# Kernel tuning notes

Hardware: AMD Instinct MI355X
Metric: run time of the kernel (lower is better)

## Reference

```python
import jax, jax.numpy as jnp
import numpy as np

DIM = 2048
NHEAD = 16
HEAD_DIM = DIM // NHEAD
FF_HIDDEN = 5632
EPS = 1e-6


def setup_inputs() -> dict:
    key = jax.random.key(0)
    ks = jax.random.split(key, 8)
    B, S = 2, 2048
    sd = 0.02
    return {
        "x": jax.random.normal(ks[0], (B, S, DIM), dtype=jnp.float32),
        "w_qkv": jax.random.normal(ks[1], (DIM, 3 * DIM), dtype=jnp.float32) * sd,
        "w_out": jax.random.normal(ks[2], (DIM, DIM), dtype=jnp.float32) * sd,
        "g1": jnp.ones((DIM,), dtype=jnp.float32),
        "g2": jnp.ones((DIM,), dtype=jnp.float32),
        "w1": jax.random.normal(ks[3], (DIM, FF_HIDDEN), dtype=jnp.float32) * sd,
        "w3": jax.random.normal(ks[4], (DIM, FF_HIDDEN), dtype=jnp.float32) * sd,
        "w2": jax.random.normal(ks[5], (FF_HIDDEN, DIM), dtype=jnp.float32) * sd,
    }


def _rmsnorm(x, g):
    rms = jnp.sqrt(jnp.mean(x * x, axis=-1, keepdims=True) + EPS)
    return x / rms * g


def _attention(x, w_qkv, w_out):
    B, S, D = x.shape
    qkv = x @ w_qkv  # [B,S,3D]
    q, k, v = jnp.split(qkv, 3, axis=-1)
    # [B,H,S,hd]
    q = q.reshape(B, S, NHEAD, HEAD_DIM).transpose(0, 2, 1, 3)
    k = k.reshape(B, S, NHEAD, HEAD_DIM).transpose(0, 2, 1, 3)
    v = v.reshape(B, S, NHEAD, HEAD_DIM).transpose(0, 2, 1, 3)
    scores = jnp.einsum("bhqd,bhkd->bhqk", q, k) / jnp.sqrt(jnp.float32(HEAD_DIM))
    causal = jnp.tril(jnp.ones((S, S), dtype=bool))
    scores = jnp.where(causal, scores, -jnp.inf)
    attn = jax.nn.softmax(scores, axis=-1)
    out = jnp.einsum("bhqk,bhkd->bhqd", attn, v)
    out = out.transpose(0, 2, 1, 3).reshape(B, S, D)
    return out @ w_out


def _swiglu(x, w1, w3, w2):
    return (jax.nn.silu(x @ w1) * (x @ w3)) @ w2


def reference(x, w_qkv, w_out, g1, g2, w1, w3, w2):
    x = x + _attention(_rmsnorm(x, g1), w_qkv, w_out)
    x = x + _swiglu(_rmsnorm(x, g2), w1, w3, w2)
    return x
```

## Files before the change

kernel.cpp:

```cpp
#include <hip/hip_runtime.h>
#include <hip/hip_bf16.h>
#include <stdint.h>


typedef __attribute__((ext_vector_type(8))) short bf16x8;
typedef __attribute__((ext_vector_type(8))) unsigned short u16x8;
typedef __attribute__((ext_vector_type(4))) float f32x4;

__device__ __forceinline__ unsigned short f2bf(float f) {
  union { float f; unsigned int u; } c; c.f = f;
  unsigned int u = c.u + 0x7fffu + ((c.u >> 16) & 1u);
  return (unsigned short)(u >> 16);
}
__device__ __forceinline__ float bf2f(unsigned short h) {
  union { unsigned int u; float f; } c; c.u = ((unsigned int)h) << 16;
  return c.f;
}

__device__ __forceinline__ void gload16(const void* g, void* l) {
  __builtin_amdgcn_global_load_lds(
      (const __attribute__((address_space(1))) void*)g,
      (__attribute__((address_space(3))) void*)l, 16, 0, 0);
}

__global__ __launch_bounds__(256)
void rmsnorm_bf16(const float* __restrict__ x, const float* __restrict__ g,
                  unsigned short* __restrict__ y)
{
  const long row = blockIdx.x;
  const float* xr = x + row * 2048;
  const int t = threadIdx.x;
  float4 a = *(const float4*)(xr + t * 8);
  float4 b = *(const float4*)(xr + t * 8 + 4);
  float ss = a.x*a.x + a.y*a.y + a.z*a.z + a.w*a.w
           + b.x*b.x + b.y*b.y + b.z*b.z + b.w*b.w;
#pragma unroll
  for (int off = 32; off >= 1; off >>= 1) ss += __shfl_xor(ss, off, 64);
  __shared__ float sm[4];
  if ((t & 63) == 0) sm[t >> 6] = ss;
  __syncthreads();
  float inv = rsqrtf((sm[0] + sm[1] + sm[2] + sm[3]) * (1.0f / 2048.0f) + 1e-6f);
  float4 ga = *(const float4*)(g + t * 8);
  float4 gb = *(const float4*)(g + t * 8 + 4);
  u16x8 ov;
  ov[0] = f2bf(a.x * inv * ga.x); ov[1] = f2bf(a.y * inv * ga.y);
  ov[2] = f2bf(a.z * inv * ga.z); ov[3] = f2bf(a.w * inv * ga.w);
  ov[4] = f2bf(b.x * inv * gb.x); ov[5] = f2bf(b.y * inv * gb.y);
  ov[6] = f2bf(b.z * inv * gb.z); ov[7] = f2bf(b.w * inv * gb.w);
  *(u16x8*)(y + row * 2048 + t * 8) = ov;
}

__global__ __launch_bounds__(256)
void rmsnorm_bf16_in(const unsigned short* __restrict__ x, const float* __restrict__ g,
                     unsigned short* __restrict__ y)
{
  const long row = blockIdx.x;
  const unsigned short* xr = x + row * 2048;
  const int t = threadIdx.x;
  u16x8 iv = *(const u16x8*)(xr + t * 8);
  float v[8];
  float ss = 0.f;
#pragma unroll
  for (int j = 0; j < 8; j++) { v[j] = bf2f(iv[j]); ss += v[j] * v[j]; }
#pragma unroll
  for (int off = 32; off >= 1; off >>= 1) ss += __shfl_xor(ss, off, 64);
  __shared__ float sm[4];
  if ((t & 63) == 0) sm[t >> 6] = ss;
  __syncthreads();
  float inv = rsqrtf((sm[0] + sm[1] + sm[2] + sm[3]) * (1.0f / 2048.0f) + 1e-6f);
  float4 ga = *(const float4*)(g + t * 8);
  float4 gb = *(const float4*)(g + t * 8 + 4);
  u16x8 ov;
  ov[0] = f2bf(v[0] * inv * ga.x); ov[1] = f2bf(v[1] * inv * ga.y);
  ov[2] = f2bf(v[2] * inv * ga.z); ov[3] = f2bf(v[3] * inv * ga.w);
  ov[4] = f2bf(v[4] * inv * gb.x); ov[5] = f2bf(v[5] * inv * gb.y);
  ov[6] = f2bf(v[6] * inv * gb.z); ov[7] = f2bf(v[7] * inv * gb.w);
  *(u16x8*)(y + row * 2048 + t * 8) = ov;
}

__global__ __launch_bounds__(256)
void transpose_w(const float* __restrict__ in, unsigned short* __restrict__ outp,
                 int K, int N)
{
  __shared__ unsigned short tile[64 * 64];
  const int n0 = blockIdx.x * 64, k0 = blockIdx.y * 64;
  const int tid = threadIdx.x;
#pragma unroll
  for (int p = 0; p < 4; p++) {
    int f = tid + p * 256;
    int row = f >> 4, c4 = f & 15;
    float4 v = *(const float4*)(in + (long)(k0 + row) * N + n0 + c4 * 4);
    ushort4 o;
    o.x = f2bf(v.x); o.y = f2bf(v.y); o.z = f2bf(v.z); o.w = f2bf(v.w);
    *(ushort4*)((char*)tile + row * 128
                + (((c4 >> 1) ^ (row >> 3)) * 16) + (c4 & 1) * 8) = o;
  }
  __syncthreads();
#pragma unroll
  for (int q = 0; q < 2; q++) {
    int idx = tid + q * 256;
    int nl = idx >> 3, l8 = idx & 7;
    u16x8 o;
#pragma unroll
    for (int j = 0; j < 8; j++) {
      int kl = l8 * 8 + j;
      o[j] = *(const unsigned short*)((char*)tile + kl * 128
               + (((nl >> 3) ^ (kl >> 3)) * 16) + (nl & 7) * 2);
    }
    *(u16x8*)(outp + (long)(n0 + nl) * K + k0 + l8 * 8) = o;
  }
}

template<int EPI>
__global__ __launch_bounds__(256)
void gemm_bt(const unsigned short* __restrict__ A,
             const unsigned short* __restrict__ Bt,
             void* __restrict__ Cout,
             const float* __restrict__ res,
             const unsigned short* __restrict__ mulsrc,
             unsigned short* __restrict__ vTout,
             int M, int N, int K)
{
  __shared__ unsigned short lds[2 * 128 * 64];
  const int tid = threadIdx.x;
  const int lane = tid & 63, wave = tid >> 6;
  const int wr = wave >> 1, wc = wave & 1;
  const int l15 = lane & 15, lg = lane >> 4;

  const int nwg = gridDim.x * gridDim.y;
  int wg = blockIdx.y * gridDim.x + blockIdx.x;
  wg = (wg & 7) * (nwg >> 3) + (wg >> 3);
  const int bx = wg % gridDim.x, by = wg / gridDim.x;
  const long m0 = (long)by * 128, n0 = (long)bx * 128;

  f32x4 acc[4][4];
#pragma unroll
  for (int m = 0; m < 4; m++)
#pragma unroll
    for (int n = 0; n < 4; n++) acc[m][n] = f32x4{0.f, 0.f, 0.f, 0.f};

  const int rsub = lane >> 3;
  const int csw = (lane & 7) ^ rsub;
  const unsigned short* Ab = A + (m0 + wave * 32 + rsub) * (long)K + csw * 8;
  const unsigned short* Bb = Bt + (n0 + wave * 32 + rsub) * (long)K + csw * 8;
  unsigned short* Al = lds + wave * 2048;
  unsigned short* Bl = lds + 8192 + wave * 2048;

  for (int kt = 0; kt < K; kt += 64) {
    __syncthreads();
#pragma unroll
    for (int i = 0; i < 4; i++) {
      gload16(Ab + (long)(i * 8) * K + kt, Al + i * 512);
      gload16(Bb + (long)(i * 8) * K + kt, Bl + i * 512);
    }
    __syncthreads();
#pragma unroll
    for (int kc = 0; kc < 2; kc++) {
      bf16x8 af[4], bfr[4];
#pragma unroll
      for (int m = 0; m < 4; m++) {
        int row = wr * 64 + m * 16 + l15;
        int off = row * 128 + ((kc * 64 + lg * 16) ^ ((row & 7) << 4));
        af[m] = *(const bf16x8*)((const char*)lds + off);
      }
#pragma unroll
      for (int n = 0; n < 4; n++) {
        int row = wc * 64 + n * 16 + l15;
        int off = 16384 + row * 128 + ((kc * 64 + lg * 16) ^ ((row & 7) << 4));
        bfr[n] = *(const bf16x8*)((const char*)lds + off);
      }
#pragma unroll
      for (int m = 0; m < 4; m++)
#pragma unroll
        for (int n = 0; n < 4; n++)
          acc[m][n] = __builtin_amdgcn_mfma_f32_16x16x32_bf16(af[m], bfr[n], acc[m][n], 0, 0, 0);
    }
  }

  if (EPI == 3) {
#pragma unroll
    for (int m = 0; m < 4; m++)
#pragma unroll
      for (int n = 0; n < 4; n++)
#pragma unroll
        for (int r = 0; r < 4; r++) {
          long row = m0 + wr * 64 + m * 16 + lg * 4 + r;
          long col = n0 + wc * 64 + n * 16 + l15;
          ((float*)Cout)[row * N + col] = acc[m][n][r] + res[row * N + col];
        }
    return;
  }

  __syncthreads();
  unsigned short* Cl = lds;
#pragma unroll
  for (int m = 0; m < 4; m++)
#pragma unroll
    for (int n = 0; n < 4; n++)
#pragma unroll
      for (int r = 0; r < 4; r++) {
        float v = acc[m][n][r];
        if (EPI == 1) v = v / (1.f + __expf(-v));
        int row = wr * 64 + m * 16 + lg * 4 + r;
        int col = wc * 64 + n * 16 + l15;
        Cl[row * 128 + (((col >> 3) ^ (row >> 3)) & 15) * 8 + (col & 7)] = f2bf(v);
      }
  __syncthreads();
#pragma unroll
  for (int r8 = 0; r8 < 8; r8++) {
    int id = tid + r8 * 256;
    int row = id >> 4, c = (id & 15) * 8;
    int ch = (id & 15) ^ (row >> 3);
    long grow = m0 + row, gcol = n0 + c;
    u16x8 v = *(const u16x8*)(Cl + row * 128 + ch * 8);
    if (EPI == 2) {
      u16x8 mm = *(const u16x8*)(mulsrc + grow * N + gcol);
#pragma unroll
      for (int j = 0; j < 8; j++) v[j] = f2bf(bf2f(v[j]) * bf2f(mm[j]));
    }
    *(u16x8*)((unsigned short*)Cout + grow * N + gcol) = v;
  }

  if (EPI == 0 && vTout != nullptr && n0 >= 4096) {
    const int hh = (int)((n0 - 4096) >> 7);
    const int b = (int)(m0 >> 11);
    const long s0 = m0 & 2047;
    unsigned short* vtb = vTout + ((long)(b * 16 + hh) * 128) * 2048;
#pragma unroll
    for (int r8 = 0; r8 < 8; r8++) {
      int id = tid + r8 * 256;
      int d = id >> 4, sc = (id & 15) * 8;
      int ch = ((d >> 3) ^ (id & 15)) & 15;
      u16x8 v;
#pragma unroll
      for (int j = 0; j < 8; j++) v[j] = Cl[(sc + j) * 128 + ch * 8 + (d & 7)];
      *(u16x8*)(vtb + (long)d * 2048 + s0 + sc) = v;
    }
  }
}

template<int EPI>
__global__ __launch_bounds__(256)
void gemm_mt64(const unsigned short* __restrict__ A,
               const unsigned short* __restrict__ Bt,
               void* __restrict__ Cout,
               const float* __restrict__ res,
               const unsigned short* __restrict__ res16,
               int M, int N, int K)
{
  __shared__ unsigned short lds[64 * 64 + 128 * 64];
  const int tid = threadIdx.x;
  const int lane = tid & 63, wave = tid >> 6;
  const int wr = wave >> 1, wc = wave & 1;
  const int l15 = lane & 15, lg = lane >> 4;

  const int nwg = gridDim.x * gridDim.y;
  int wg = blockIdx.y * gridDim.x + blockIdx.x;
  wg = (wg & 7) * (nwg >> 3) + (wg >> 3);
  const int bx = wg % gridDim.x, by = wg / gridDim.x;
  const long m0 = (long)by * 64, n0 = (long)bx * 128;

  f32x4 acc[2][4];
#pragma unroll
  for (int m = 0; m < 2; m++)
#pragma unroll
    for (int n = 0; n < 4; n++) acc[m][n] = f32x4{0.f, 0.f, 0.f, 0.f};

  const int rsub = lane >> 3;
  const int csw = (lane & 7) ^ rsub;
  const unsigned short* Ab = A + (m0 + wave * 16 + rsub) * (long)K + csw * 8;
  const unsigned short* Bb = Bt + (n0 + wave * 32 + rsub) * (long)K + csw * 8;
  unsigned short* Al = lds + wave * 1024;
  unsigned short* Bl = lds + 4096 + wave * 2048;

  for (int kt = 0; kt < K; kt += 64) {
    __syncthreads();
#pragma unroll
    for (int i = 0; i < 2; i++)
      gload16(Ab + (long)(i * 8) * K + kt, Al + i * 512);
#pragma unroll
    for (int i = 0; i < 4; i++)
      gload16(Bb + (long)(i * 8) * K + kt, Bl + i * 512);
    __syncthreads();
#pragma unroll
    for (int kc = 0; kc < 2; kc++) {
      bf16x8 af[2], bfr[4];
#pragma unroll
      for (int m = 0; m < 2; m++) {
        int row = wr * 32 + m * 16 + l15;
        int off = row * 128 + ((kc * 64 + lg * 16) ^ ((row & 7) << 4));
        af[m] = *(const bf16x8*)((const char*)lds + off);
      }
#pragma unroll
      for (int n = 0; n < 4; n++) {
        int row = wc * 64 + n * 16 + l15;
        int off = 8192 + row * 128 + ((kc * 64 + lg * 16) ^ ((row & 7) << 4));
        bfr[n] = *(const bf16x8*)((const char*)lds + off);
      }
#pragma unroll
      for (int m = 0; m < 2; m++)
#pragma unroll
        for (int n = 0; n < 4; n++)
          acc[m][n] = __builtin_amdgcn_mfma_f32_16x16x32_bf16(af[m], bfr[n], acc[m][n], 0, 0, 0);
    }
  }

  if (EPI == 5) {
#pragma unroll
    for (int m = 0; m < 2; m++)
#pragma unroll
      for (int n = 0; n < 4; n++)
#pragma unroll
        for (int r = 0; r < 4; r++) {
          long row = m0 + wr * 32 + m * 16 + lg * 4 + r;
          long col = n0 + wc * 64 + n * 16 + l15;
          ((float*)Cout)[row * N + col] = acc[m][n][r] + bf2f(res16[row * N + col]);
        }
    return;
  }

  __syncthreads();
  unsigned short* Cl = lds;
#pragma unroll
  for (int m = 0; m < 2; m++)
#pragma unroll
    for (int n = 0; n < 4; n++)
#pragma unroll
      for (int r = 0; r < 4; r++) {
        int row = wr * 32 + m * 16 + lg * 4 + r;
        int col = wc * 64 + n * 16 + l15;
        float v = acc[m][n][r] + res[(m0 + row) * N + n0 + col];
        Cl[row * 128 + (((col >> 3) ^ (row >> 3)) & 15) * 8 + (col & 7)] = f2bf(v);
      }
  __syncthreads();
#pragma unroll
  for (int rnd = 0; rnd < 4; rnd++) {
    int id = tid + rnd * 256;
    int row = id >> 4, c = (id & 15) * 8;
    int ch = (id & 15) ^ (row >> 3);
    u16x8 v = *(const u16x8*)(Cl + row * 128 + ch * 8);
    *(u16x8*)((unsigned short*)Cout + (m0 + row) * N + n0 + c) = v;
  }
}

#define QSTEP(qf, mrow, lrow, o, qb, isdiag) do {                              \
    f32x4 sacc[4];                                                             \
    __builtin_amdgcn_s_setprio(1);                                             \
    _Pragma("unroll")                                                          \
    for (int cg = 0; cg < 4; cg++) {                                           \
      f32x4 a = f32x4{0.f, 0.f, 0.f, 0.f};                                     \
      _Pragma("unroll")                                                        \
      for (int kc = 0; kc < 4; kc++) {                                         \
        int krow = cg * 16 + l15;                                              \
        bf16x8 kf = *(const bf16x8*)((char*)Klds +                             \
            (krow * 256 + ((kc * 64 + lg * 16) ^ ((krow & 7) << 4))));         \
        a = __builtin_amdgcn_mfma_f32_16x16x32_bf16(qf[kc], kf, a, 0, 0, 0);   \
      }                                                                        \
      sacc[cg] = a;                                                            \
    }                                                                          \
    __builtin_amdgcn_s_setprio(0);                                             \
    float p[4][4], pm[4];                                                      \
    _Pragma("unroll")                                                          \
    for (int r = 0; r < 4; r++) pm[r] = -1e30f;                                \
    _Pragma("unroll")                                                          \
    for (int cg = 0; cg < 4; cg++)                                             \
      _Pragma("unroll")                                                        \
      for (int r = 0; r < 4; r++) {                                            \
        float v = sacc[cg][r] * scale;                                         \
        if (isdiag) {                                                          \
          int kvg = kv0 + cg * 16 + l15;                                       \
          int qg = qb + w * 16 + lg * 4 + r;                                   \
          if (kvg > qg) v = -1e30f;                                            \
        }                                                                      \
        p[cg][r] = v;                                                          \
        pm[r] = fmaxf(pm[r], v);                                               \
      }                                                                        \
    _Pragma("unroll")                                                          \
    for (int r = 0; r < 4; r++) {                                              \
      _Pragma("unroll")                                                        \
      for (int off = 1; off < 16; off <<= 1)                                   \
        pm[r] = fmaxf(pm[r], __shfl_xor(pm[r], off, 64));                      \
      float mn = fmaxf(mrow[r], pm[r]);                                        \
      float al = __expf(mrow[r] - mn);                                         \
      mrow[r] = mn;                                                            \
      float s = 0.f;                                                           \
      _Pragma("unroll")                                                        \
      for (int cg = 0; cg < 4; cg++) { p[cg][r] = __expf(p[cg][r] - mn); s += p[cg][r]; } \
      _Pragma("unroll")                                                        \
      for (int off = 1; off < 16; off <<= 1)                                   \
        s += __shfl_xor(s, off, 64);                                           \
      lrow[r] = lrow[r] * al + s;                                              \
      _Pragma("unroll")                                                        \
      for (int dg = 0; dg < 8; dg++) o[dg][r] *= al;                           \
    }                                                                          \
    _Pragma("unroll")                                                          \
    for (int cg = 0; cg < 4; cg++)                                             \
      _Pragma("unroll")                                                        \
      for (int r = 0; r < 4; r++) {                                            \
        int q = lg * 4 + r;                                                    \
        *((unsigned short*)((char*)&Plds[w][0] +                               \
            (q * 128 + (((cg * 16 + l15) * 2) ^ ((q & 7) << 4))))) = f2bf(p[cg][r]); \
      }                                                                        \
    asm volatile("s_waitcnt lgkmcnt(0)" ::: "memory");                         \
    __builtin_amdgcn_sched_barrier(0);                                         \
    __builtin_amdgcn_s_setprio(1);                                             \
    _Pragma("unroll")                                                          \
    for (int kc = 0; kc < 2; kc++) {                                           \
      bf16x8 pa = *(const bf16x8*)((char*)&Plds[w][0] +                        \
          (l15 * 128 + ((kc * 64 + lg * 16) ^ ((l15 & 7) << 4))));             \
      _Pragma("unroll")                                                        \
      for (int dg = 0; dg < 8; dg++) {                                         \
        int d = dg * 16 + l15;                                                 \
        bf16x8 vf = *(const bf16x8*)((char*)Vlds +                             \
            (d * 128 + ((kc * 64 + lg * 16) ^ ((d & 7) << 4))));               \
        o[dg] = __builtin_amdgcn_mfma_f32_16x16x32_bf16(pa, vf, o[dg], 0, 0, 0); \
      }                                                                        \
    }                                                                          \
    __builtin_amdgcn_s_setprio(0);                                             \
  } while (0)

__global__ __launch_bounds__(256, 2)
void attn_fwd(const unsigned short* __restrict__ qkv,
              const unsigned short* __restrict__ vT,
              unsigned short* __restrict__ out)
{
  __shared__ unsigned short Klds[64 * 128];
  __shared__ unsigned short Vlds[128 * 64];
  __shared__ unsigned short Plds[4][16 * 64];
  const int tid = threadIdx.x, lane = tid & 63, w = tid >> 6;
  const int l15 = lane & 15, lg = lane >> 4;

  const int nwg = gridDim.x * gridDim.y;
  int wg = blockIdx.y * gridDim.x + blockIdx.x;
  wg = (wg & 7) * (nwg >> 3) + (wg >> 3);
  const int ip = wg % 16;
  const int bh = wg / 16;
  const int b = bh >> 4, hh = bh & 15;

  const int qbA = ip * 64, qbB = (31 - ip) * 64;
  const long base = (long)b * 2048 * 6144;
  const int qoff = hh * 128, koff = 2048 + hh * 128;
  const unsigned short* vTg = vT + (long)bh * (128 * 2048);

  bf16x8 qfA[4], qfB[4];
  {
    long qrA = qbA + w * 16 + l15, qrB = qbB + w * 16 + l15;
#pragma unroll
    for (int kc = 0; kc < 4; kc++) {
      qfA[kc] = *(const bf16x8*)(qkv + base + qrA * 6144 + qoff + kc * 32 + lg * 8);
      qfB[kc] = *(const bf16x8*)(qkv + base + qrB * 6144 + qoff + kc * 32 + lg * 8);
    }
  }
  f32x4 oA[8], oB[8];
#pragma unroll
  for (int dg = 0; dg < 8; dg++) {
    oA[dg] = f32x4{0.f, 0.f, 0.f, 0.f};
    oB[dg] = f32x4{0.f, 0.f, 0.f, 0.f};
  }
  float mA[4] = {-1e30f, -1e30f, -1e30f, -1e30f}, lA[4] = {0.f, 0.f, 0.f, 0.f};
  float mB[4] = {-1e30f, -1e30f, -1e30f, -1e30f}, lB[4] = {0.f, 0.f, 0.f, 0.f};
  const float scale = 0.08838834764831845f;

  const int s_st = tid >> 4, d0 = (tid & 15) * 8;
  const int vrow = tid >> 3, vc = tid & 7;

  const int nt = 32 - ip;
  for (int t = 0; t < nt; t++) {
    const int kv0 = t * 64;
#pragma unroll
    for (int u = 0; u < 4; u++) {
      int srow = s_st + u * 16;
      uint4 kk = *(const uint4*)(qkv + base + (long)(kv0 + srow) * 6144 + koff + d0);
      *(uint4*)((char*)Klds + (srow * 256 + ((d0 * 2) ^ ((srow & 7) << 4)))) = kk;
    }
#pragma unroll
    for (int u = 0; u < 4; u++) {
      int d = vrow + u * 32;
      uint4 vv = *(const uint4*)(vTg + (long)d * 2048 + kv0 + vc * 8);
      *(uint4*)((char*)Vlds + (d * 128 + ((vc * 16) ^ ((d & 7) << 4)))) = vv;
    }
    __syncthreads();

    if (t <= ip) QSTEP(qfA, mA, lA, oA, qbA, (t == ip));
    QSTEP(qfB, mB, lB, oB, qbB, (t == nt - 1));

    __syncthreads();
  }

#pragma unroll
  for (int r = 0; r < 4; r++) {
    float invA = 1.f / lA[r], invB = 1.f / lB[r];
    long rowA = (long)b * 2048 + qbA + w * 16 + lg * 4 + r;
    long rowB = (long)b * 2048 + qbB + w * 16 + lg * 4 + r;
#pragma unroll
    for (int dg = 0; dg < 8; dg++) {
      out[rowA * 2048 + hh * 128 + dg * 16 + l15] = f2bf(oA[dg][r] * invA);
      out[rowB * 2048 + hh * 128 + dg * 16 + l15] = f2bf(oB[dg][r] * invB);
    }
  }
}

extern "C" void kernel_launch(void* const* d_in, const int* in_sizes, int n_in,
                              void* d_out, int out_size, void* d_ws, size_t ws_size,
                              hipStream_t stream)
{
  const float* x     = (const float*)d_in[0];
  const float* w_qkv = (const float*)d_in[1];
  const float* w_out = (const float*)d_in[2];
  const float* g1    = (const float*)d_in[3];
  const float* g2    = (const float*)d_in[4];
  const float* w1    = (const float*)d_in[5];
  const float* w3    = (const float*)d_in[6];
  const float* w2    = (const float*)d_in[7];
  float* outp = (float*)d_out;
  char* ws = (char*)d_ws;

  unsigned short* wT  = (unsigned short*)(ws);
  unsigned short* y   = (unsigned short*)(ws + 25165824);
  unsigned short* qkv = (unsigned short*)(ws + 41943040);
  unsigned short* att = (unsigned short*)(ws + 92274688);
  unsigned short* x1b = (unsigned short*)(ws + 109051904);
  unsigned short* s1  = (unsigned short*)(ws + 142606336);
  unsigned short* vTb = s1;
  unsigned short* h   = qkv;

  rmsnorm_bf16<<<4096, 256, 0, stream>>>(x, g1, y);
  transpose_w<<<dim3(96, 32), 256, 0, stream>>>(w_qkv, wT, 2048, 6144);
  gemm_bt<0><<<dim3(48, 32), 256, 0, stream>>>(y, wT, qkv, nullptr, nullptr, vTb, 4096, 6144, 2048);
  attn_fwd<<<dim3(16, 32), 256, 0, stream>>>(qkv, vTb, att);
  transpose_w<<<dim3(32, 32), 256, 0, stream>>>(w_out, wT, 2048, 2048);
  gemm_mt64<4><<<dim3(16, 64), 256, 0, stream>>>(att, wT, x1b, x, nullptr, 4096, 2048, 2048);

  rmsnorm_bf16_in<<<4096, 256, 0, stream>>>(x1b, g2, y);
  transpose_w<<<dim3(88, 32), 256, 0, stream>>>(w1, wT, 2048, 5632);
  gemm_bt<1><<<dim3(44, 32), 256, 0, stream>>>(y, wT, s1, nullptr, nullptr, nullptr, 4096, 5632, 2048);
  transpose_w<<<dim3(88, 32), 256, 0, stream>>>(w3, wT, 2048, 5632);
  gemm_bt<2><<<dim3(44, 32), 256, 0, stream>>>(y, wT, h, nullptr, s1, nullptr, 4096, 5632, 2048);
  transpose_w<<<dim3(32, 88), 256, 0, stream>>>(w2, wT, 5632, 2048);
  gemm_mt64<5><<<dim3(16, 64), 256, 0, stream>>>(h, wT, outp, nullptr, x1b, 4096, 2048, 5632);
}
```

Baseline: 702.6 us.

## Replace 128x128 GEMM with 256x256 eight-wave double-buffered pipelined GEMM

Replaces the 128x128 single-buffered gemm_bt with a 256x256-tile, 512-thread kernel that double-buffers A and B in 128KB LDS. It interleaves global-to-LDS loads with MFMA phases using explicit barriers, waitcnts, sched_barriers and setprio. The goal is to hide global load latency and raise arithmetic intensity for the QKV, w1 and w3 GEMMs. In exchange it runs at one workgroup per CU with a large register footprint, and the smaller grids (384 and 352 blocks) may not balance evenly across CUs.

```diff
diff --git a/kernel.cpp b/kernel.cpp
--- a/kernel.cpp
+++ b/kernel.cpp
@@ -111,108 +111,146 @@
   }
 }
 
+#define PH_BAR __builtin_amdgcn_s_barrier()
+#define SB0 __builtin_amdgcn_sched_barrier(0)
+#define LGKM0 asm volatile("s_waitcnt lgkmcnt(0)" ::: "memory")
+#define VM4 asm volatile("s_waitcnt vmcnt(4)" ::: "memory");
+#define VM0 asm volatile("s_waitcnt vmcnt(0)" ::: "memory");
+
+#define STGA(RBASE, h, t) { \
+  gload16(Asb + (long)((h) * 128) * K + (t) * 64, L + (RBASE) + wave * 1024); \
+  gload16(Asb + (long)((h) * 128 + 64) * K + (t) * 64, L + (RBASE) + 8192 + wave * 1024); }
+#define STGB(RBASE, h, t) { \
+  gload16(Bsb + (long)((h) * 128) * K + (t) * 64, L + (RBASE) + wave * 1024); \
+  gload16(Bsb + (long)((h) * 128 + 64) * K + (t) * 64, L + (RBASE) + 8192 + wave * 1024); }
+
+#define LDB8(RBASE) { \
+  bfr0[0] = *(const bf16x8*)(L + (RBASE) + bbase + 0 * 2048 + k0off); \
+  bfr1[0] = *(const bf16x8*)(L + (RBASE) + bbase + 0 * 2048 + k1off); \
+  bfr0[1] = *(const bf16x8*)(L + (RBASE) + bbase + 1 * 2048 + k0off); \
+  bfr1[1] = *(const bf16x8*)(L + (RBASE) + bbase + 1 * 2048 + k1off); \
+  bfr0[2] = *(const bf16x8*)(L + (RBASE) + bbase + 2 * 2048 + k0off); \
+  bfr1[2] = *(const bf16x8*)(L + (RBASE) + bbase + 2 * 2048 + k1off); \
+  bfr0[3] = *(const bf16x8*)(L + (RBASE) + bbase + 3 * 2048 + k0off); \
+  bfr1[3] = *(const bf16x8*)(L + (RBASE) + bbase + 3 * 2048 + k1off); }
+
+#define NOP_
+
+#define PHASE(RAc, mg, PRE, STGOP, GATE) { \
+  bf16x8 a00, a01, a10, a11; \
+  a00 = *(const bf16x8*)(L + (RAc) + abase + (mg) * 2048 + k0off); \
+  a01 = *(const bf16x8*)(L + (RAc) + abase + (mg) * 2048 + k1off); \
+  a10 = *(const bf16x8*)(L + (RAc) + abase + ((mg) + 1) * 2048 + k0off); \
+  a11 = *(const bf16x8*)(L + (RAc) + abase + ((mg) + 1) * 2048 + k1off); \
+  PRE STGOP \
+  SB0; PH_BAR; LGKM0; SB0; \
+  __builtin_amdgcn_s_setprio(1); \
+  _Pragma("unroll") \
+  for (int n = 0; n < 4; n++) { \
+    acc[(mg)][n]     = __builtin_amdgcn_mfma_f32_16x16x32_bf16(a00, bfr0[n], acc[(mg)][n], 0, 0, 0); \
+    acc[(mg)][n]     = __builtin_amdgcn_mfma_f32_16x16x32_bf16(a01, bfr1[n], acc[(mg)][n], 0, 0, 0); \
+    acc[(mg) + 1][n] = __builtin_amdgcn_mfma_f32_16x16x32_bf16(a10, bfr0[n], acc[(mg) + 1][n], 0, 0, 0); \
+    acc[(mg) + 1][n] = __builtin_amdgcn_mfma_f32_16x16x32_bf16(a11, bfr1[n], acc[(mg) + 1][n], 0, 0, 0); } \
+  __builtin_amdgcn_s_setprio(0); SB0; \
+  GATE PH_BAR; SB0; }
+
 template<int EPI>
-__global__ __launch_bounds__(256)
-void gemm_bt(const unsigned short* __restrict__ A,
+__global__ __launch_bounds__(512, 1)
+void gemm256(const unsigned short* __restrict__ A,
              const unsigned short* __restrict__ Bt,
              void* __restrict__ Cout,
-             const float* __restrict__ res,
              const unsigned short* __restrict__ mulsrc,
              unsigned short* __restrict__ vTout,
              int M, int N, int K)
 {
-  __shared__ unsigned short lds[2 * 128 * 64];
+  __shared__ alignas(16) char L[131072];
   const int tid = threadIdx.x;
   const int lane = tid & 63, wave = tid >> 6;
-  const int wr = wave >> 1, wc = wave & 1;
+  const int wr = wave >> 2, wc = wave & 3;
   const int l15 = lane & 15, lg = lane >> 4;
 
   const int nwg = gridDim.x * gridDim.y;
   int wg = blockIdx.y * gridDim.x + blockIdx.x;
   wg = (wg & 7) * (nwg >> 3) + (wg >> 3);
   const int bx = wg % gridDim.x, by = wg / gridDim.x;
-  const long m0 = (long)by * 128, n0 = (long)bx * 128;
-
-  f32x4 acc[4][4];
-#pragma unroll
-  for (int m = 0; m < 4; m++)
+  const long m0 = (long)by * 256, n0 = (long)bx * 256;
+
+  f32x4 acc[8][4];
+#pragma unroll
+  for (int m = 0; m < 8; m++)
 #pragma unroll
     for (int n = 0; n < 4; n++) acc[m][n] = f32x4{0.f, 0.f, 0.f, 0.f};
 
-  const int rsub = lane >> 3;
-  const int csw = (lane & 7) ^ rsub;
-  const unsigned short* Ab = A + (m0 + wave * 32 + rsub) * (long)K + csw * 8;
-  const unsigned short* Bb = Bt + (n0 + wave * 32 + rsub) * (long)K + csw * 8;
-  unsigned short* Al = lds + wave * 2048;
-  unsigned short* Bl = lds + 8192 + wave * 2048;
-
-  for (int kt = 0; kt < K; kt += 64) {
-    __syncthreads();
-#pragma unroll
-    for (int i = 0; i < 4; i++) {
-      gload16(Ab + (long)(i * 8) * K + kt, Al + i * 512);
-      gload16(Bb + (long)(i * 8) * K + kt, Bl + i * 512);
-    }
-    __syncthreads();
-#pragma unroll
-    for (int kc = 0; kc < 2; kc++) {
-      bf16x8 af[4], bfr[4];
-#pragma unroll
-      for (int m = 0; m < 4; m++) {
-        int row = wr * 64 + m * 16 + l15;
-        int off = row * 128 + ((kc * 64 + lg * 16) ^ ((row & 7) << 4));
-        af[m] = *(const bf16x8*)((const char*)lds + off);
-      }
-#pragma unroll
-      for (int n = 0; n < 4; n++) {
-        int row = wc * 64 + n * 16 + l15;
-        int off = 16384 + row * 128 + ((kc * 64 + lg * 16) ^ ((row & 7) << 4));
-        bfr[n] = *(const bf16x8*)((const char*)lds + off);
-      }
-#pragma unroll
-      for (int m = 0; m < 4; m++)
-#pragma unroll
-        for (int n = 0; n < 4; n++)
-          acc[m][n] = __builtin_amdgcn_mfma_f32_16x16x32_bf16(af[m], bfr[n], acc[m][n], 0, 0, 0);
-    }
-  }
-
-  if (EPI == 3) {
-#pragma unroll
-    for (int m = 0; m < 4; m++)
-#pragma unroll
-      for (int n = 0; n < 4; n++)
-#pragma unroll
-        for (int r = 0; r < 4; r++) {
-          long row = m0 + wr * 64 + m * 16 + lg * 4 + r;
-          long col = n0 + wc * 64 + n * 16 + l15;
-          ((float*)Cout)[row * N + col] = acc[m][n][r] + res[row * N + col];
-        }
-    return;
-  }
-
-  __syncthreads();
-  unsigned short* Cl = lds;
-#pragma unroll
-  for (int m = 0; m < 4; m++)
+  const int r0 = tid >> 3, c0 = tid & 7;
+  const int csw = c0 ^ (r0 & 7);
+  const unsigned short* Asb = A + (m0 + r0) * (long)K + csw * 8;
+  const unsigned short* Bsb = Bt + (n0 + r0) * (long)K + csw * 8;
+
+  const int x = (l15 & 7) << 4;
+  const int k0off = (lg * 16) ^ x;
+  const int k1off = (64 + lg * 16) ^ x;
+  const int abase = l15 * 128;
+  const int bbase = ((wc & 1) * 64 + l15) * 128;
+
+  const int RA_r0 = wr * 16384;
+  const int RB_r0 = 32768 + (wc >> 1) * 16384;
+  const int RA_r1 = 65536 + RA_r0;
+  const int RB_r1 = 65536 + RB_r0;
+
+  bf16x8 bfr0[4], bfr1[4];
+
+  const int nkt = K >> 6, nit = nkt >> 1;
+
+  STGA(0, 0, 0) STGA(16384, 1, 0)
+  STGB(32768, 0, 0) STGB(32768 + 16384, 1, 0)
+  STGB(65536 + 32768, 0, 1) STGB(65536 + 32768 + 16384, 1, 1)
+  VM4 PH_BAR; SB0;
+
+  for (int it = 0; it < nit - 1; ++it) {
+    const int t1 = 2 * it + 1, t2 = t1 + 1, t3 = t1 + 2;
+    PHASE(RA_r0, 0, LDB8(RB_r0), STGA(65536, 0, t1), NOP_)
+    PHASE(RA_r0, 2, NOP_, STGA(65536 + 16384, 1, t1), NOP_)
+    PHASE(RA_r0, 4, NOP_, STGB(32768, 0, t2), NOP_)
+    PHASE(RA_r0, 6, NOP_, STGB(32768 + 16384, 1, t2), VM4)
+    PHASE(RA_r1, 0, LDB8(RB_r1), STGA(0, 0, t2), NOP_)
+    PHASE(RA_r1, 2, NOP_, STGA(16384, 1, t2), NOP_)
+    PHASE(RA_r1, 4, NOP_, STGB(65536 + 32768, 0, t3), NOP_)
+    PHASE(RA_r1, 6, NOP_, STGB(65536 + 32768 + 16384, 1, t3), VM4)
+  }
+  {
+    const int t1 = nkt - 1;
+    PHASE(RA_r0, 0, LDB8(RB_r0), STGA(65536, 0, t1), NOP_)
+    PHASE(RA_r0, 2, NOP_, STGA(65536 + 16384, 1, t1), NOP_)
+    PHASE(RA_r0, 4, NOP_, NOP_, NOP_)
+    PHASE(RA_r0, 6, NOP_, NOP_, VM0)
+    PHASE(RA_r1, 0, LDB8(RB_r1), NOP_, NOP_)
+    PHASE(RA_r1, 2, NOP_, NOP_, NOP_)
+    PHASE(RA_r1, 4, NOP_, NOP_, NOP_)
+    PHASE(RA_r1, 6, NOP_, NOP_, NOP_)
+  }
+
+  __syncthreads();
+  unsigned short* Cl = (unsigned short*)L;
+#pragma unroll
+  for (int m = 0; m < 8; m++)
 #pragma unroll
     for (int n = 0; n < 4; n++)
 #pragma unroll
       for (int r = 0; r < 4; r++) {
         float v = acc[m][n][r];
         if (EPI == 1) v = v / (1.f + __expf(-v));
-        int row = wr * 64 + m * 16 + lg * 4 + r;
+        int row = wr * 128 + m * 16 + lg * 4 + r;
         int col = wc * 64 + n * 16 + l15;
-        Cl[row * 128 + (((col >> 3) ^ (row >> 3)) & 15) * 8 + (col & 7)] = f2bf(v);
+        Cl[row * 256 + (((col >> 3) ^ (row >> 3)) & 31) * 8 + (col & 7)] = f2bf(v);
       }
   __syncthreads();
 #pragma unroll
-  for (int r8 = 0; r8 < 8; r8++) {
-    int id = tid + r8 * 256;
-    int row = id >> 4, c = (id & 15) * 8;
-    int ch = (id & 15) ^ (row >> 3);
+  for (int rnd = 0; rnd < 16; rnd++) {
+    int id = tid + rnd * 512;
+    int row = id >> 5, c = (id & 31) * 8;
+    int ch = (id & 31) ^ ((row >> 3) & 31);
     long grow = m0 + row, gcol = n0 + c;
-    u16x8 v = *(const u16x8*)(Cl + row * 128 + ch * 8);
+    u16x8 v = *(const u16x8*)(Cl + row * 256 + ch * 8);
     if (EPI == 2) {
       u16x8 mm = *(const u16x8*)(mulsrc + grow * N + gcol);
 #pragma unroll
@@ -222,19 +260,21 @@
   }
 
   if (EPI == 0 && vTout != nullptr && n0 >= 4096) {
-    const int hh = (int)((n0 - 4096) >> 7);
+    const int hbase = (int)((n0 - 4096) >> 7);
     const int b = (int)(m0 >> 11);
     const long s0 = m0 & 2047;
-    unsigned short* vtb = vTout + ((long)(b * 16 + hh) * 128) * 2048;
-#pragma unroll
-    for (int r8 = 0; r8 < 8; r8++) {
-      int id = tid + r8 * 256;
-      int d = id >> 4, sc = (id & 15) * 8;
-      int ch = ((d >> 3) ^ (id & 15)) & 15;
+#pragma unroll
+    for (int rnd = 0; rnd < 16; rnd++) {
+      int id = tid + rnd * 512;
+      int col = id >> 5, sc8 = (id & 31) * 8;
+      int ch = ((col >> 3) ^ (id & 31)) & 31;
       u16x8 v;
 #pragma unroll
-      for (int j = 0; j < 8; j++) v[j] = Cl[(sc + j) * 128 + ch * 8 + (d & 7)];
-      *(u16x8*)(vtb + (long)d * 2048 + s0 + sc) = v;
+      for (int j = 0; j < 8; j++)
+        v[j] = Cl[(sc8 + j) * 256 + ch * 8 + (col & 7)];
+      int head = col >> 7, d = col & 127;
+      unsigned short* vtb = vTout + ((long)((b * 16 + hbase + head) * 128 + d)) * 2048;
+      *(u16x8*)(vtb + s0 + sc8) = v;
     }
   }
 }
@@ -526,16 +566,16 @@
 
   rmsnorm_bf16<<<4096, 256, 0, stream>>>(x, g1, y);
   transpose_w<<<dim3(96, 32), 256, 0, stream>>>(w_qkv, wT, 2048, 6144);
-  gemm_bt<0><<<dim3(48, 32), 256, 0, stream>>>(y, wT, qkv, nullptr, nullptr, vTb, 4096, 6144, 2048);
+  gemm256<0><<<dim3(24, 16), 512, 0, stream>>>(y, wT, qkv, nullptr, vTb, 4096, 6144, 2048);
   attn_fwd<<<dim3(16, 32), 256, 0, stream>>>(qkv, vTb, att);
   transpose_w<<<dim3(32, 32), 256, 0, stream>>>(w_out, wT, 2048, 2048);
   gemm_mt64<4><<<dim3(16, 64), 256, 0, stream>>>(att, wT, x1b, x, nullptr, 4096, 2048, 2048);
 
   rmsnorm_bf16_in<<<4096, 256, 0, stream>>>(x1b, g2, y);
   transpose_w<<<dim3(88, 32), 256, 0, stream>>>(w1, wT, 2048, 5632);
-  gemm_bt<1><<<dim3(44, 32), 256, 0, stream>>>(y, wT, s1, nullptr, nullptr, nullptr, 4096, 5632, 2048);
+  gemm256<1><<<dim3(22, 16), 512, 0, stream>>>(y, wT, s1, nullptr, nullptr, 4096, 5632, 2048);
   transpose_w<<<dim3(88, 32), 256, 0, stream>>>(w3, wT, 2048, 5632);
-  gemm_bt<2><<<dim3(44, 32), 256, 0, stream>>>(y, wT, h, nullptr, s1, nullptr, 4096, 5632, 2048);
+  gemm256<2><<<dim3(22, 16), 512, 0, stream>>>(y, wT, h, s1, nullptr, 4096, 5632, 2048);
   transpose_w<<<dim3(32, 88), 256, 0, stream>>>(w2, wT, 5632, 2048);
   gemm_mt64<5><<<dim3(16, 64), 256, 0, stream>>>(h, wT, outp, nullptr, x1b, 4096, 2048, 5632);
 }
```

Result: slower. 737.2 us (+4.9%).
